# Kernel tuning notes

Measured on AMD Instinct MI355X. Metric: run time of the kernel, lower is better.

## Reference

```python
import jax, jax.numpy as jnp
import numpy as np

TRUNC = 2.0  # NSFP truncated chamfer: squared dists >= 2 are zeroed


def _mlp(x, W0, b0, Wh, bh, Wl, bl):
    h = jax.nn.relu(x @ W0 + b0)
    for i in range(Wh.shape[0]):
        h = jax.nn.relu(h @ Wh[i] + bh[i])
    return h @ Wl + bl


def _chamfer(x, y):
    d = (jnp.sum(x * x, axis=1)[:, None]
         + jnp.sum(y * y, axis=1)[None, :]
         - 2.0 * (x @ y.T))
    dx = jnp.min(d, axis=1)  # [N] NN dist x->y
    dy = jnp.min(d, axis=0)  # [M] NN dist y->x
    dx = jnp.where(dx < TRUNC, dx, 0.0)
    dy = jnp.where(dy < TRUNC, dy, 0.0)
    return jnp.mean(dx) + jnp.mean(dy)


def setup_inputs() -> dict:
    key = jax.random.key(0)
    ks = jax.random.split(key, 16)
    N = 20000
    F = 128
    H = 7  # hidden 128->128 layers (layer_size=8)
    s_in = 1.0 / np.sqrt(3.0)
    s_h = 1.0 / np.sqrt(F)
    d = {
        'pc0': jax.random.normal(ks[0], (N, 3), jnp.float32) * 10.0,
        'pc1': jax.random.normal(ks[1], (N, 3), jnp.float32) * 10.0,
        'W0': jax.random.normal(ks[2], (3, F), jnp.float32) * s_in,
        'b0': jnp.zeros((F,), jnp.float32),
        'Wh': jax.random.normal(ks[3], (H, F, F), jnp.float32) * s_h,
        'bh': jnp.zeros((H, F), jnp.float32),
        'Wl': jax.random.normal(ks[4], (F, 3), jnp.float32) * s_h,
        'bl': jnp.zeros((3,), jnp.float32),
        'W0i': jax.random.normal(ks[5], (3, F), jnp.float32) * s_in,
        'b0i': jnp.zeros((F,), jnp.float32),
        'Whi': jax.random.normal(ks[6], (H, F, F), jnp.float32) * s_h,
        'bhi': jnp.zeros((H, F), jnp.float32),
        'Wli': jax.random.normal(ks[7], (F, 3), jnp.float32) * s_h,
        'bli': jnp.zeros((3,), jnp.float32),
    }
    return d


def reference(pc0, pc1, W0, b0, Wh, bh, Wl, bl,
              W0i, b0i, Whi, bhi, Wli, bli):
    forward_flow = _mlp(pc0, W0, b0, Wh, bh, Wl, bl)          # [N,3]
    pc0_to_pc1 = pc0 + forward_flow
    inverse_flow = _mlp(pc0_to_pc1, W0i, b0i, Whi, bhi, Wli, bli)
    est_pc1_to_pc0 = pc0_to_pc1 - inverse_flow
    forward_loss = _chamfer(pc0_to_pc1, pc1)
    inverse_loss = _chamfer(est_pc1_to_pc0, pc0)
    return forward_loss + inverse_loss


if __name__ == '__main__':
    out = reference(**setup_inputs())
    print(out)
```

## Files before the change

### kernel.cpp

```cpp
#include <hip/hip_runtime.h>
#include <hip/hip_bf16.h>

#define F 128
#define NHID 7
#define BP 80
#define NPT 5
#define TRUNC_ 2.0f

#define GM 32
#define GM3 (GM * GM * GM)
#define GLO (-28.0f)
#define CELL 1.75f
#define GINV (1.0f / 1.75f)
#define SCAN_BLKS (GM3 / 256)
#define NGRID 4
#define PACKB 896
#define ZB (NGRID * GM3 / 256)
#define BQ 128

typedef __attribute__((ext_vector_type(8))) short short8v;
typedef __attribute__((ext_vector_type(4))) float f32x4;

__device__ inline unsigned short f2bf(float v)
{
    __hip_bfloat16 b = __float2bfloat16(v);
    return __builtin_bit_cast(unsigned short, b);
}
__device__ inline float bf2f(unsigned short u)
{
    unsigned int x = ((unsigned int)u) << 16;
    return __builtin_bit_cast(float, x);
}

__device__ inline int hsw(int row, int col)
{
    return row * 128 + ((((col >> 3) ^ (row & 7)) << 3) | (col & 7));
}

__device__ inline void barrier_nd()
{
    asm volatile("s_waitcnt lgkmcnt(0)" ::: "memory");
    __builtin_amdgcn_s_barrier();
}

__global__ __launch_bounds__(256) void prep_kernel(
    const float* __restrict__ Wh, const float* __restrict__ Whi,
    const float* __restrict__ Wl, const float* __restrict__ Wli,
    unsigned short* __restrict__ whp, unsigned short* __restrict__ wlp,
    float* __restrict__ wlt, int* __restrict__ counts, unsigned int* __restrict__ done)
{
    int bid = blockIdx.x;
    int t = threadIdx.x;
    if (bid < PACKB) {
        int idx = bid * 256 + t;
        int j = idx & 7;
        int l = (idx >> 3) & 63;
        int tt = (idx >> 9) & 7;
        int s = (idx >> 12) & 3;
        int m = idx >> 14;
        int k = s * 32 + (l >> 4) * 8 + j;
        int c = tt * 16 + (l & 15);
        const float* W = (m < 7 ? Wh + (size_t)m * F * F
                                : Whi + (size_t)(m - 7) * F * F);
        float w = W[k * F + c];
        unsigned short hi = f2bf(w);
        unsigned short lo = f2bf(w - bf2f(hi));
        whp[idx] = hi;
        wlp[idx] = lo;
    } else if (bid < PACKB + ZB) {
        counts[(bid - PACKB) * 256 + t] = 0;
    } else {
#pragma unroll
        for (int r = 0; r < 3; ++r) {
            int e = r * 256 + t;
            int mI = e / 384;
            int rem = e - mI * 384;
            int c = rem >> 7;
            int k = rem & 127;
            const float* W = mI ? Wli : Wl;
            wlt[e] = W[k * 3 + c];
        }
        if (t == 0) *done = 0u;
    }
}

__device__ inline int cell_of(float x, float y, float z)
{
    int cx = (int)floorf((x - GLO) * GINV);
    int cy = (int)floorf((y - GLO) * GINV);
    int cz = (int)floorf((z - GLO) * GINV);
    cx = min(max(cx, 0), GM - 1);
    cy = min(max(cy, 0), GM - 1);
    cz = min(max(cz, 0), GM - 1);
    return (cz * GM + cy) * GM + cx;
}

__global__ __launch_bounds__(512, 2) void mlp_fused_kernel(
    const float* __restrict__ pc0, const float* __restrict__ pc1,
    const float* __restrict__ W0a, const float* __restrict__ b0a,
    const float* __restrict__ W0b, const float* __restrict__ b0b,
    const unsigned short* __restrict__ whp,
    const unsigned short* __restrict__ wlp,
    const float* __restrict__ bha, const float* __restrict__ bhb,
    const float* __restrict__ wlt,
    const float* __restrict__ bla, const float* __restrict__ blb,
    float* __restrict__ Aout, float* __restrict__ Cout,
    int* __restrict__ counts, int N)
{
    __shared__ unsigned short hX[BP * 128];
    __shared__ unsigned short hY[BP * 128];
    __shared__ float Al[BP][4];
    __shared__ float Cl[BP][4];

    const int tid = threadIdx.x;
    const int lane = tid & 63;
    const int wv = tid >> 6;
    const int arow = lane & 15;
    const int kg = lane >> 4;
    const int p0 = blockIdx.x * BP;

    unsigned short* cur = hX;
    unsigned short* nxt = hY;

    short8v wAhi, wAlo, wBhi, wBlo;
    short8v hA[NPT], hB[NPT];

#define LW(WHI, WLO, LI, S) { \
        size_t off = ((size_t)(((LI) * 4 + (S)) * 8 + wv) * 64 + lane) * 8; \
        WHI = *(const short8v*)(whp + off); \
        WLO = *(const short8v*)(wlp + off); }
#define LH(D, S) { _Pragma("unroll") for (int p = 0; p < NPT; ++p) \
        D[p] = *(const short8v*)&cur[hsw(p * 16 + arow, (S) * 32 + kg * 8)]; }
#define MM(WHI, WLO, H) { \
    _Pragma("unroll") for (int p = 0; p < NPT; ++p) \
        acc[p] = __builtin_amdgcn_mfma_f32_16x16x32_bf16(WHI, H[p], acc[p], 0, 0, 0); \
    _Pragma("unroll") for (int p = 0; p < NPT; ++p) \
        acc[p] = __builtin_amdgcn_mfma_f32_16x16x32_bf16(WLO, H[p], acc[p], 0, 0, 0); }

    LW(wAhi, wAlo, 0, 0)
    LW(wBhi, wBlo, 0, 1)
    __builtin_amdgcn_sched_barrier(0);

    for (int M = 0; M < 2; ++M) {
        const float* W0 = M ? W0b : W0a;
        const float* b0 = M ? b0b : b0a;
        const float* bh = M ? bhb : bha;
        const float* bl = M ? blb : bla;

        {
            const int jg = tid & 31;
            const int pgg = tid >> 5;
            const int j0 = jg * 4;
            float4 wr0 = *(const float4*)(W0 + 0 * F + j0);
            float4 wr1 = *(const float4*)(W0 + 1 * F + j0);
            float4 wr2 = *(const float4*)(W0 + 2 * F + j0);
            float4 bb0 = *(const float4*)(b0 + j0);
#pragma unroll
            for (int p = 0; p < 5; ++p) {
                int pt = pgg * 5 + p;
                float x0, x1, x2;
                if (M == 0) {
                    int gp = p0 + pt;
                    int cp = gp < N ? gp : N - 1;
                    x0 = pc0[cp * 3 + 0]; x1 = pc0[cp * 3 + 1]; x2 = pc0[cp * 3 + 2];
                } else {
                    x0 = Al[pt][0]; x1 = Al[pt][1]; x2 = Al[pt][2];
                }
                float hx = fmaxf(fmaf(x0, wr0.x, fmaf(x1, wr1.x, fmaf(x2, wr2.x, bb0.x))), 0.f);
                float hy = fmaxf(fmaf(x0, wr0.y, fmaf(x1, wr1.y, fmaf(x2, wr2.y, bb0.y))), 0.f);
                float hz = fmaxf(fmaf(x0, wr0.z, fmaf(x1, wr1.z, fmaf(x2, wr2.z, bb0.z))), 0.f);
                float hw = fmaxf(fmaf(x0, wr0.w, fmaf(x1, wr1.w, fmaf(x2, wr2.w, bb0.w))), 0.f);
                short4 hv = make_short4((short)f2bf(hx), (short)f2bf(hy),
                                        (short)f2bf(hz), (short)f2bf(hw));
                *(short4*)&cur[hsw(pt, j0)] = hv;
            }
        }
        barrier_nd();

        for (int l = 0; l < NHID; ++l) {
            const int L = M * 7 + l;
            const int Ln = (L + 1 < 14) ? (L + 1) : 13;
            f32x4 acc[NPT];
            {
                float4 b4 = *(const float4*)&bh[l * F + wv * 16 + kg * 4];
#pragma unroll
                for (int p = 0; p < NPT; ++p)
                    acc[p] = (f32x4){b4.x, b4.y, b4.z, b4.w};
            }

            LH(hA, 0) LH(hB, 1)
            __builtin_amdgcn_sched_barrier(0);
            MM(wAhi, wAlo, hA)
            LW(wAhi, wAlo, L, 2) LH(hA, 2)
            __builtin_amdgcn_sched_barrier(0);
            MM(wBhi, wBlo, hB)
            LW(wBhi, wBlo, L, 3) LH(hB, 3)
            __builtin_amdgcn_sched_barrier(0);
            MM(wAhi, wAlo, hA)
            LW(wAhi, wAlo, Ln, 0)
            __builtin_amdgcn_sched_barrier(0);
            MM(wBhi, wBlo, hB)
            LW(wBhi, wBlo, Ln, 1)

#pragma unroll
            for (int p = 0; p < NPT; ++p) {
                float v0 = fmaxf(acc[p][0], 0.f), v1 = fmaxf(acc[p][1], 0.f);
                float v2 = fmaxf(acc[p][2], 0.f), v3 = fmaxf(acc[p][3], 0.f);
                short4 hv = make_short4((short)f2bf(v0), (short)f2bf(v1),
                                        (short)f2bf(v2), (short)f2bf(v3));
                *(short4*)&nxt[hsw(p * 16 + arow, wv * 16 + kg * 4)] = hv;
            }
            barrier_nd();
            unsigned short* tsw = cur; cur = nxt; nxt = tsw;
        }

        if (tid < 240) {
            int pt = tid / 3;
            int c = tid - 3 * pt;
            const float* wl = wlt + M * 384 + c * 128;
            float a0 = 0.f, a1 = 0.f, a2 = 0.f, a3 = 0.f;
#pragma unroll
            for (int q = 0; q < 16; ++q) {
                short8v h8 = *(const short8v*)&cur[hsw(pt, q * 8)];
                float4 wa = *(const float4*)(wl + q * 8);
                float4 wb = *(const float4*)(wl + q * 8 + 4);
                a0 = fmaf(bf2f((unsigned short)h8[0]), wa.x, a0);
                a1 = fmaf(bf2f((unsigned short)h8[1]), wa.y, a1);
                a2 = fmaf(bf2f((unsigned short)h8[2]), wa.z, a2);
                a3 = fmaf(bf2f((unsigned short)h8[3]), wa.w, a3);
                a0 = fmaf(bf2f((unsigned short)h8[4]), wb.x, a0);
                a1 = fmaf(bf2f((unsigned short)h8[5]), wb.y, a1);
                a2 = fmaf(bf2f((unsigned short)h8[6]), wb.z, a2);
                a3 = fmaf(bf2f((unsigned short)h8[7]), wb.w, a3);
            }
            float flow = ((a0 + a1) + (a2 + a3)) + bl[c];
            int gp = p0 + pt;
            int cp = gp < N ? gp : N - 1;
            if (M == 0) {
                float val = pc0[cp * 3 + c] + flow;
                Al[pt][c] = val;
                if (gp < N) Aout[gp * 3 + c] = val;
            } else {
                float val = Al[pt][c] - flow;
                Cl[pt][c] = val;
                if (gp < N) Cout[gp * 3 + c] = val;
            }
        }
        barrier_nd();
    }
#undef LW
#undef LH
#undef MM

    if (tid < BP) {
        int gp = p0 + tid;
        if (gp < N) {
            atomicAdd(&counts[1 * GM3 + cell_of(Al[tid][0], Al[tid][1], Al[tid][2])], 1);
            atomicAdd(&counts[3 * GM3 + cell_of(Cl[tid][0], Cl[tid][1], Cl[tid][2])], 1);
            atomicAdd(&counts[0 * GM3 + cell_of(pc1[gp * 3 + 0], pc1[gp * 3 + 1], pc1[gp * 3 + 2])], 1);
            atomicAdd(&counts[2 * GM3 + cell_of(pc0[gp * 3 + 0], pc0[gp * 3 + 1], pc0[gp * 3 + 2])], 1);
        }
    }
}

__device__ inline const float* cloud_ptr(int g, const float* g0, const float* g1,
                                         const float* g2, const float* g3)
{
    return g == 0 ? g0 : (g == 1 ? g1 : (g == 2 ? g2 : g3));
}

__global__ __launch_bounds__(256) void scan1(
    const int* __restrict__ counts, int* __restrict__ offs, int* __restrict__ bsum)
{
    int tid = threadIdx.x;
    int i = blockIdx.x * 256 + tid;
    int v = counts[i];
    __shared__ int s[256];
    s[tid] = v;
    __syncthreads();
#pragma unroll
    for (int off = 1; off < 256; off <<= 1) {
        int t = (tid >= off) ? s[tid - off] : 0;
        __syncthreads();
        s[tid] += t;
        __syncthreads();
    }
    offs[i] = s[tid] - v;
    if (tid == 255) bsum[blockIdx.x] = s[255];
}

__global__ __launch_bounds__(256) void scan23(
    int* __restrict__ offs, const int* __restrict__ bsum, int* __restrict__ counts)
{
    int seg = blockIdx.x / SCAN_BLKS;
    int pos = blockIdx.x - seg * SCAN_BLKS;
    const int* bs = bsum + seg * SCAN_BLKS;
    int t = threadIdx.x;
    int v = (t < pos) ? bs[t] : 0;
    __shared__ int red[4];
#pragma unroll
    for (int o = 32; o > 0; o >>= 1) v += __shfl_down(v, o, 64);
    if ((t & 63) == 0) red[t >> 6] = v;
    __syncthreads();
    int prefix = red[0] + red[1] + red[2] + red[3];
    int i = blockIdx.x * 256 + t;
    offs[i] += prefix;
    counts[i] = 0;
}

__global__ __launch_bounds__(256) void grid_fill(
    const float* __restrict__ B, const float* __restrict__ A,
    const float* __restrict__ D, const float* __restrict__ C,
    const int* __restrict__ offs, int* __restrict__ counts,
    float4* __restrict__ pts, int n)
{
    int g = blockIdx.y;
    const float* P = cloud_ptr(g, B, A, D, C);
    int i = blockIdx.x * 256 + threadIdx.x;
    if (i < n) {
        float x = P[i * 3 + 0], y = P[i * 3 + 1], z = P[i * 3 + 2];
        int c = g * GM3 + cell_of(x, y, z);
        int slot = offs[c] + atomicAdd(&counts[c], 1);
        pts[(size_t)g * n + slot] = make_float4(x, y, z, 0.f);
    }
}

__device__ inline float block_sum256(float v)
{
    __shared__ float sws[4];
#pragma unroll
    for (int o = 32; o > 0; o >>= 1) v += __shfl_down(v, o, 64);
    int w = threadIdx.x >> 6;
    if ((threadIdx.x & 63) == 0) sws[w] = v;
    __syncthreads();
    if (threadIdx.x == 0) v = sws[0] + sws[1] + sws[2] + sws[3];
    return v;
}

__device__ inline float boxd1(float q, int c)
{
    float lo = GLO + c * CELL;
    return fmaxf(fmaxf(lo - q, q - (lo + CELL)), 0.f);
}

__global__ __launch_bounds__(256) void grid_search(
    const int* __restrict__ offs, const int* __restrict__ counts,
    const float4* __restrict__ pts, float* __restrict__ partials,
    unsigned int* __restrict__ done, float* __restrict__ out, float inv, int n)
{
    const int d = blockIdx.y;
    const float4* Qs = pts + (size_t)(d ^ 1) * n;
    const float4* P  = pts + (size_t)d * n;
    const int* ofs = offs + (size_t)d * GM3;
    const int* cnt = counts + (size_t)d * GM3;

    const int tid = threadIdx.x;
    const int ql = tid & (BQ - 1);
    const int half = tid >> 7;
    const int i = blockIdx.x * BQ + ql;

    float mn = 3.4e38f;
    if (i < n) {
        float4 q = Qs[i];
        int cx = min(max((int)floorf((q.x - GLO) * GINV), 0), GM - 1);
        int cy = min(max((int)floorf((q.y - GLO) * GINV), 0), GM - 1);
        int cz = min(max((int)floorf((q.z - GLO) * GINV), 0), GM - 1);
        int xcl = max(cx - 1, 0), xch = min(cx + 1, GM - 1);
        int r0 = half * 4;

        int o[5], e[5];
#pragma unroll
        for (int r = 0; r < 5; ++r) {
            o[r] = 0; e[r] = 0;
            bool act = half ? true : (r < 4);
            if (act) {
                int rr = r0 + r;
                int dz = rr / 3, dy = rr - dz * 3;
                int z = cz + dz - 1;
                int y = cy + dy - 1;
                if ((unsigned)z < GM && (unsigned)y < GM) {
                    float dzd = boxd1(q.z, z);
                    float dyd = boxd1(q.y, y);
                    float dyz2 = fmaf(dzd, dzd, dyd * dyd);
                    if (dyz2 < TRUNC_) {
                        float rx = sqrtf(TRUNC_ - dyz2);
                        int xlo = max((int)floorf((q.x - rx - GLO) * GINV), xcl);
                        int xhi = min((int)floorf((q.x + rx - GLO) * GINV), xch);
                        if (xlo <= xhi) {
                            int rowbase = (z * GM + y) * GM;
                            o[r] = ofs[rowbase + xlo];
                            e[r] = ofs[rowbase + xhi] + cnt[rowbase + xhi];
                        }
                    }
                }
            }
        }
#pragma unroll
        for (int r = 0; r < 5; ++r) {
            for (int k = o[r]; k < e[r]; ++k) {
                float4 p = P[k];
                float ddx = q.x - p.x, ddy = q.y - p.y, ddz = q.z - p.z;
                mn = fminf(mn, fmaf(ddx, ddx, fmaf(ddy, ddy, ddz * ddz)));
            }
        }
    }

    __shared__ float m0[BQ];
    if (half == 0) m0[ql] = mn;
    __syncthreads();
    float val = 0.f;
    if (half == 1 && i < n) {
        float m = fminf(mn, m0[ql]);
        val = (m < TRUNC_) ? m : 0.f;
    }
    float bs = block_sum256(val);

    __shared__ int lastflag;
    if (threadIdx.x == 0) {
        atomicExch(&partials[(size_t)d * gridDim.x + blockIdx.x], bs);
        __threadfence();
        unsigned v = atomicAdd(done, 1u);
        lastflag = (v == (unsigned)(NGRID * gridDim.x - 1)) ? 1 : 0;
    }
    __syncthreads();
    if (lastflag) {
        int NPt = NGRID * gridDim.x;
        float s = 0.f;
        for (int j = threadIdx.x; j < NPt; j += 256)
            s += atomicAdd(&partials[j], 0.0f);
        __syncthreads();
        float tot = block_sum256(s);
        if (threadIdx.x == 0) out[0] = tot * inv;
    }
}

extern "C" void kernel_launch(void* const* d_in, const int* in_sizes, int n_in,
                              void* d_out, int out_size, void* d_ws, size_t ws_size,
                              hipStream_t stream)
{
    const float* pc0 = (const float*)d_in[0];
    const float* pc1 = (const float*)d_in[1];
    const float* W0  = (const float*)d_in[2];
    const float* b0  = (const float*)d_in[3];
    const float* Wh  = (const float*)d_in[4];
    const float* bh  = (const float*)d_in[5];
    const float* Wl  = (const float*)d_in[6];
    const float* bl  = (const float*)d_in[7];
    const float* W0i = (const float*)d_in[8];
    const float* b0i = (const float*)d_in[9];
    const float* Whi = (const float*)d_in[10];
    const float* bhi = (const float*)d_in[11];
    const float* Wli = (const float*)d_in[12];
    const float* bli = (const float*)d_in[13];
    float* out = (float*)d_out;

    const int N = in_sizes[0] / 3;

    char* base = (char*)d_ws;
    float*  A        = (float*)(base + 0);
    float*  C        = (float*)(base + 240000);
    int*    counts   = (int*)  (base + 480000);
    int*    offs     = (int*)  (base + 1004288);
    int*    bsum     = (int*)  (base + 1528576);
    float4* pts      = (float4*)(base + 1532672);
    float*  partials = (float*)(base + 2812672);
    unsigned int* done = (unsigned int*)(base + 2816768);
    unsigned short* whp = (unsigned short*)(base + 2816784);
    unsigned short* wlp = (unsigned short*)(base + 3275536);
    float*  wlt      = (float*)(base + 3734288);

    const int PB = (N + 255) / 256;
    const int QB = (N + BQ - 1) / BQ;

    hipLaunchKernelGGL(prep_kernel, dim3(PACKB + ZB + 1), dim3(256), 0, stream,
                       Wh, Whi, Wl, Wli, whp, wlp, wlt, counts, done);

    int mlpg = (N + BP - 1) / BP;
    hipLaunchKernelGGL(mlp_fused_kernel, dim3(mlpg), dim3(512), 0, stream,
                       pc0, pc1, W0, b0, W0i, b0i, whp, wlp, bh, bhi,
                       wlt, bl, bli, A, C, counts, N);

    hipLaunchKernelGGL(scan1, dim3(ZB), dim3(256), 0, stream, counts, offs, bsum);
    hipLaunchKernelGGL(scan23, dim3(ZB), dim3(256), 0, stream, offs, bsum, counts);
    hipLaunchKernelGGL(grid_fill, dim3(PB, NGRID), dim3(256), 0, stream,
                       pc1, A, pc0, C, offs, counts, pts, N);

    hipLaunchKernelGGL(grid_search, dim3(QB, NGRID), dim3(256), 0, stream,
                       offs, counts, pts, partials, done, out,
                       1.0f / (float)N, N);
}
```

Measured before the change: 78.54 us.

## Fuse scan, grid fill and grid search into one persistent kernel with grid barriers

Replaces the four post-MLP kernels (two-stage scan, grid fill, neighbour search) with a single kernel whose phases are separated by software grid-wide barriers built on atomic counters. The aim is to remove three kernel launches and the idle gaps between dependent stages. In exchange, all 4*QB blocks must be resident at once or the spin barriers deadlock, and every barrier adds spin and fence overhead. Launch bounds request three blocks per CU to make co-residency more likely.

```diff
diff --git a/kernel.cpp b/kernel.cpp
--- a/kernel.cpp
+++ b/kernel.cpp
@@ -43,11 +43,24 @@
     __builtin_amdgcn_s_barrier();
 }
 
+__device__ inline void gbar(unsigned int* ctr, unsigned int target)
+{
+    __syncthreads();
+    if (threadIdx.x == 0) {
+        __threadfence();
+        atomicAdd(ctr, 1u);
+        while (atomicAdd(ctr, 0u) < target)
+            __builtin_amdgcn_s_sleep(4);
+        __threadfence();
+    }
+    __syncthreads();
+}
+
 __global__ __launch_bounds__(256) void prep_kernel(
     const float* __restrict__ Wh, const float* __restrict__ Whi,
     const float* __restrict__ Wl, const float* __restrict__ Wli,
     unsigned short* __restrict__ whp, unsigned short* __restrict__ wlp,
-    float* __restrict__ wlt, int* __restrict__ counts, unsigned int* __restrict__ done)
+    float* __restrict__ wlt, int* __restrict__ counts, unsigned int* __restrict__ syncv)
 {
     int bid = blockIdx.x;
     int t = threadIdx.x;
@@ -80,7 +93,7 @@
             const float* W = mI ? Wli : Wl;
             wlt[e] = W[k * 3 + c];
         }
-        if (t == 0) *done = 0u;
+        if (t < 8) syncv[t] = 0u;
     }
 }
 
@@ -269,62 +282,6 @@
     return g == 0 ? g0 : (g == 1 ? g1 : (g == 2 ? g2 : g3));
 }
 
-__global__ __launch_bounds__(256) void scan1(
-    const int* __restrict__ counts, int* __restrict__ offs, int* __restrict__ bsum)
-{
-    int tid = threadIdx.x;
-    int i = blockIdx.x * 256 + tid;
-    int v = counts[i];
-    __shared__ int s[256];
-    s[tid] = v;
-    __syncthreads();
-#pragma unroll
-    for (int off = 1; off < 256; off <<= 1) {
-        int t = (tid >= off) ? s[tid - off] : 0;
-        __syncthreads();
-        s[tid] += t;
-        __syncthreads();
-    }
-    offs[i] = s[tid] - v;
-    if (tid == 255) bsum[blockIdx.x] = s[255];
-}
-
-__global__ __launch_bounds__(256) void scan23(
-    int* __restrict__ offs, const int* __restrict__ bsum, int* __restrict__ counts)
-{
-    int seg = blockIdx.x / SCAN_BLKS;
-    int pos = blockIdx.x - seg * SCAN_BLKS;
-    const int* bs = bsum + seg * SCAN_BLKS;
-    int t = threadIdx.x;
-    int v = (t < pos) ? bs[t] : 0;
-    __shared__ int red[4];
-#pragma unroll
-    for (int o = 32; o > 0; o >>= 1) v += __shfl_down(v, o, 64);
-    if ((t & 63) == 0) red[t >> 6] = v;
-    __syncthreads();
-    int prefix = red[0] + red[1] + red[2] + red[3];
-    int i = blockIdx.x * 256 + t;
-    offs[i] += prefix;
-    counts[i] = 0;
-}
-
-__global__ __launch_bounds__(256) void grid_fill(
-    const float* __restrict__ B, const float* __restrict__ A,
-    const float* __restrict__ D, const float* __restrict__ C,
-    const int* __restrict__ offs, int* __restrict__ counts,
-    float4* __restrict__ pts, int n)
-{
-    int g = blockIdx.y;
-    const float* P = cloud_ptr(g, B, A, D, C);
-    int i = blockIdx.x * 256 + threadIdx.x;
-    if (i < n) {
-        float x = P[i * 3 + 0], y = P[i * 3 + 1], z = P[i * 3 + 2];
-        int c = g * GM3 + cell_of(x, y, z);
-        int slot = offs[c] + atomicAdd(&counts[c], 1);
-        pts[(size_t)g * n + slot] = make_float4(x, y, z, 0.f);
-    }
-}
-
 __device__ inline float block_sum256(float v)
 {
     __shared__ float sws[4];
@@ -343,94 +300,153 @@
     return fmaxf(fmaxf(lo - q, q - (lo + CELL)), 0.f);
 }
 
-__global__ __launch_bounds__(256) void grid_search(
-    const int* __restrict__ offs, const int* __restrict__ counts,
-    const float4* __restrict__ pts, float* __restrict__ partials,
-    unsigned int* __restrict__ done, float* __restrict__ out, float inv, int n)
-{
-    const int d = blockIdx.y;
-    const float4* Qs = pts + (size_t)(d ^ 1) * n;
-    const float4* P  = pts + (size_t)d * n;
-    const int* ofs = offs + (size_t)d * GM3;
-    const int* cnt = counts + (size_t)d * GM3;
-
-    const int tid = threadIdx.x;
-    const int ql = tid & (BQ - 1);
-    const int half = tid >> 7;
-    const int i = blockIdx.x * BQ + ql;
-
-    float mn = 3.4e38f;
-    if (i < n) {
-        float4 q = Qs[i];
-        int cx = min(max((int)floorf((q.x - GLO) * GINV), 0), GM - 1);
-        int cy = min(max((int)floorf((q.y - GLO) * GINV), 0), GM - 1);
-        int cz = min(max((int)floorf((q.z - GLO) * GINV), 0), GM - 1);
-        int xcl = max(cx - 1, 0), xch = min(cx + 1, GM - 1);
-        int r0 = half * 4;
-
-        int o[5], e[5];
-#pragma unroll
-        for (int r = 0; r < 5; ++r) {
-            o[r] = 0; e[r] = 0;
-            bool act = half ? true : (r < 4);
-            if (act) {
-                int rr = r0 + r;
-                int dz = rr / 3, dy = rr - dz * 3;
-                int z = cz + dz - 1;
-                int y = cy + dy - 1;
-                if ((unsigned)z < GM && (unsigned)y < GM) {
-                    float dzd = boxd1(q.z, z);
-                    float dyd = boxd1(q.y, y);
-                    float dyz2 = fmaf(dzd, dzd, dyd * dyd);
-                    if (dyz2 < TRUNC_) {
-                        float rx = sqrtf(TRUNC_ - dyz2);
-                        int xlo = max((int)floorf((q.x - rx - GLO) * GINV), xcl);
-                        int xhi = min((int)floorf((q.x + rx - GLO) * GINV), xch);
-                        if (xlo <= xhi) {
-                            int rowbase = (z * GM + y) * GM;
-                            o[r] = ofs[rowbase + xlo];
-                            e[r] = ofs[rowbase + xhi] + cnt[rowbase + xhi];
+__global__ __launch_bounds__(256, 3) void grid_pipeline(
+    const float* __restrict__ Bc, const float* __restrict__ Ac,
+    const float* __restrict__ Dc, const float* __restrict__ Cc,
+    int* __restrict__ offs, int* __restrict__ counts, int* __restrict__ bsum,
+    float4* __restrict__ pts, float* __restrict__ partials,
+    unsigned int* __restrict__ syncv, float* __restrict__ out, float inv, int n)
+{
+    const int bid = blockIdx.x;
+    const int t = threadIdx.x;
+    const unsigned int GPB = gridDim.x;
+    const int QB = (n + BQ - 1) / BQ;
+    const int PB = (n + 255) / 256;
+
+    __shared__ int s[256];
+    __shared__ float m0[BQ];
+    __shared__ int lastflag;
+
+    if (bid < ZB) {
+        int i = bid * 256 + t;
+        int v = counts[i];
+        s[t] = v;
+        __syncthreads();
+#pragma unroll
+        for (int off = 1; off < 256; off <<= 1) {
+            int x = (t >= off) ? s[t - off] : 0;
+            __syncthreads();
+            s[t] += x;
+            __syncthreads();
+        }
+        offs[i] = s[t] - v;
+        if (t == 255) bsum[bid] = s[255];
+    }
+    gbar(&syncv[0], GPB);
+
+    if (bid < ZB) {
+        int seg = bid / SCAN_BLKS;
+        int pos = bid - seg * SCAN_BLKS;
+        const int* bs = bsum + seg * SCAN_BLKS;
+        int v = (t < pos) ? bs[t] : 0;
+        __shared__ int red[4];
+#pragma unroll
+        for (int o = 32; o > 0; o >>= 1) v += __shfl_down(v, o, 64);
+        if ((t & 63) == 0) red[t >> 6] = v;
+        __syncthreads();
+        int prefix = red[0] + red[1] + red[2] + red[3];
+        int i = bid * 256 + t;
+        offs[i] += prefix;
+        counts[i] = 0;
+    }
+    gbar(&syncv[1], GPB);
+
+    if (bid < PB * NGRID) {
+        int g = bid / PB;
+        int xb = bid - g * PB;
+        const float* P = cloud_ptr(g, Bc, Ac, Dc, Cc);
+        int i = xb * 256 + t;
+        if (i < n) {
+            float x = P[i * 3 + 0], y = P[i * 3 + 1], z = P[i * 3 + 2];
+            int c = g * GM3 + cell_of(x, y, z);
+            int slot = offs[c] + atomicAdd(&counts[c], 1);
+            pts[(size_t)g * n + slot] = make_float4(x, y, z, 0.f);
+        }
+    }
+    gbar(&syncv[2], GPB);
+
+    {
+        const int d = bid / QB;
+        const int qb = bid - d * QB;
+        const float4* Qs = pts + (size_t)(d ^ 1) * n;
+        const float4* P  = pts + (size_t)d * n;
+        const int* ofs = offs + (size_t)d * GM3;
+        const int* cnt = counts + (size_t)d * GM3;
+
+        const int ql = t & (BQ - 1);
+        const int half = t >> 7;
+        const int i = qb * BQ + ql;
+
+        float mn = 3.4e38f;
+        if (i < n) {
+            float4 q = Qs[i];
+            int cx = min(max((int)floorf((q.x - GLO) * GINV), 0), GM - 1);
+            int cy = min(max((int)floorf((q.y - GLO) * GINV), 0), GM - 1);
+            int cz = min(max((int)floorf((q.z - GLO) * GINV), 0), GM - 1);
+            int xcl = max(cx - 1, 0), xch = min(cx + 1, GM - 1);
+            int r0 = half * 4;
+
+            int o[5], e[5];
+#pragma unroll
+            for (int r = 0; r < 5; ++r) {
+                o[r] = 0; e[r] = 0;
+                bool act = half ? true : (r < 4);
+                if (act) {
+                    int rr = r0 + r;
+                    int dz = rr / 3, dy = rr - dz * 3;
+                    int z = cz + dz - 1;
+                    int y = cy + dy - 1;
+                    if ((unsigned)z < GM && (unsigned)y < GM) {
+                        float dzd = boxd1(q.z, z);
+                        float dyd = boxd1(q.y, y);
+                        float dyz2 = fmaf(dzd, dzd, dyd * dyd);
+                        if (dyz2 < TRUNC_) {
+                            float rx = sqrtf(TRUNC_ - dyz2);
+                            int xlo = max((int)floorf((q.x - rx - GLO) * GINV), xcl);
+                            int xhi = min((int)floorf((q.x + rx - GLO) * GINV), xch);
+                            if (xlo <= xhi) {
+                                int rowbase = (z * GM + y) * GM;
+                                o[r] = ofs[rowbase + xlo];
+                                e[r] = ofs[rowbase + xhi] + cnt[rowbase + xhi];
+                            }
                         }
                     }
                 }
             }
-        }
-#pragma unroll
-        for (int r = 0; r < 5; ++r) {
-            for (int k = o[r]; k < e[r]; ++k) {
-                float4 p = P[k];
-                float ddx = q.x - p.x, ddy = q.y - p.y, ddz = q.z - p.z;
-                mn = fminf(mn, fmaf(ddx, ddx, fmaf(ddy, ddy, ddz * ddz)));
-            }
-        }
-    }
-
-    __shared__ float m0[BQ];
-    if (half == 0) m0[ql] = mn;
-    __syncthreads();
-    float val = 0.f;
-    if (half == 1 && i < n) {
-        float m = fminf(mn, m0[ql]);
-        val = (m < TRUNC_) ? m : 0.f;
-    }
-    float bs = block_sum256(val);
-
-    __shared__ int lastflag;
-    if (threadIdx.x == 0) {
-        atomicExch(&partials[(size_t)d * gridDim.x + blockIdx.x], bs);
-        __threadfence();
-        unsigned v = atomicAdd(done, 1u);
-        lastflag = (v == (unsigned)(NGRID * gridDim.x - 1)) ? 1 : 0;
-    }
-    __syncthreads();
-    if (lastflag) {
-        int NPt = NGRID * gridDim.x;
-        float s = 0.f;
-        for (int j = threadIdx.x; j < NPt; j += 256)
-            s += atomicAdd(&partials[j], 0.0f);
+#pragma unroll
+            for (int r = 0; r < 5; ++r) {
+                for (int k = o[r]; k < e[r]; ++k) {
+                    float4 p = P[k];
+                    float ddx = q.x - p.x, ddy = q.y - p.y, ddz = q.z - p.z;
+                    mn = fminf(mn, fmaf(ddx, ddx, fmaf(ddy, ddy, ddz * ddz)));
+                }
+            }
+        }
+
+        if (half == 0) m0[ql] = mn;
         __syncthreads();
-        float tot = block_sum256(s);
-        if (threadIdx.x == 0) out[0] = tot * inv;
+        float val = 0.f;
+        if (half == 1 && i < n) {
+            float m = fminf(mn, m0[ql]);
+            val = (m < TRUNC_) ? m : 0.f;
+        }
+        float bs = block_sum256(val);
+
+        if (t == 0) {
+            atomicExch(&partials[bid], bs);
+            __threadfence();
+            unsigned v = atomicAdd(&syncv[3], 1u);
+            lastflag = (v == GPB - 1u) ? 1 : 0;
+        }
+        __syncthreads();
+        if (lastflag) {
+            float ss = 0.f;
+            for (int j = t; j < (int)GPB; j += 256)
+                ss += atomicAdd(&partials[j], 0.0f);
+            __syncthreads();
+            float tot = block_sum256(ss);
+            if (t == 0) out[0] = tot * inv;
+        }
     }
 }
 
@@ -464,28 +480,22 @@
     int*    bsum     = (int*)  (base + 1528576);
     float4* pts      = (float4*)(base + 1532672);
     float*  partials = (float*)(base + 2812672);
-    unsigned int* done = (unsigned int*)(base + 2816768);
-    unsigned short* whp = (unsigned short*)(base + 2816784);
-    unsigned short* wlp = (unsigned short*)(base + 3275536);
-    float*  wlt      = (float*)(base + 3734288);
-
-    const int PB = (N + 255) / 256;
+    unsigned int* syncv = (unsigned int*)(base + 2816768);
+    unsigned short* whp = (unsigned short*)(base + 2816800);
+    unsigned short* wlp = (unsigned short*)(base + 3275552);
+    float*  wlt      = (float*)(base + 3734304);
+
     const int QB = (N + BQ - 1) / BQ;
 
     hipLaunchKernelGGL(prep_kernel, dim3(PACKB + ZB + 1), dim3(256), 0, stream,
-                       Wh, Whi, Wl, Wli, whp, wlp, wlt, counts, done);
+                       Wh, Whi, Wl, Wli, whp, wlp, wlt, counts, syncv);
 
     int mlpg = (N + BP - 1) / BP;
     hipLaunchKernelGGL(mlp_fused_kernel, dim3(mlpg), dim3(512), 0, stream,
                        pc0, pc1, W0, b0, W0i, b0i, whp, wlp, bh, bhi,
                        wlt, bl, bli, A, C, counts, N);
 
-    hipLaunchKernelGGL(scan1, dim3(ZB), dim3(256), 0, stream, counts, offs, bsum);
-    hipLaunchKernelGGL(scan23, dim3(ZB), dim3(256), 0, stream, offs, bsum, counts);
-    hipLaunchKernelGGL(grid_fill, dim3(PB, NGRID), dim3(256), 0, stream,
-                       pc1, A, pc0, C, offs, counts, pts, N);
-
-    hipLaunchKernelGGL(grid_search, dim3(QB, NGRID), dim3(256), 0, stream,
-                       offs, counts, pts, partials, done, out,
-                       1.0f / (float)N, N);
-}
+    hipLaunchKernelGGL(grid_pipeline, dim3(NGRID * QB), dim3(256), 0, stream,
+                       pc1, A, pc0, C, offs, counts, bsum, pts, partials,
+                       syncv, out, 1.0f / (float)N, N);
+}
```

Measured after the change: 244.8 us. 212% more time.

## Double-buffer full-layer MLP weights and split grid search into four sub-threads per query

Applied to the files above, without the earlier changes.

The MLP kernel now double-buffers all four weight slices of the next layer in registers, prefetching them during the current layer's MFMAs and fully unrolling the layer loops, so weight-load latency is hidden across layers. The grid search assigns four threads per query (3+2+2+2 cell rows) instead of two, which doubles the number of blocks and shortens the per-thread serial neighbor scan. The partials buffer grows, so the workspace offsets shift. The cost is more register pressure in the MLP kernel, which may reduce occupancy or spill, and a larger reduction in the grid search.

```diff
diff --git a/kernel.cpp b/kernel.cpp
--- a/kernel.cpp
+++ b/kernel.cpp
@@ -16,7 +16,7 @@
 #define NGRID 4
 #define PACKB 896
 #define ZB (NGRID * GM3 / 256)
-#define BQ 128
+#define QPB 64
 
 typedef __attribute__((ext_vector_type(8))) short short8v;
 typedef __attribute__((ext_vector_type(4))) float f32x4;
@@ -122,25 +122,25 @@
     unsigned short* cur = hX;
     unsigned short* nxt = hY;
 
-    short8v wAhi, wAlo, wBhi, wBlo;
+    short8v whB[2][4], wlB[2][4];
     short8v hA[NPT], hB[NPT];
 
-#define LW(WHI, WLO, LI, S) { \
+#define LWB(NB, LI, S) { \
         size_t off = ((size_t)(((LI) * 4 + (S)) * 8 + wv) * 64 + lane) * 8; \
-        WHI = *(const short8v*)(whp + off); \
-        WLO = *(const short8v*)(wlp + off); }
+        whB[NB][S] = *(const short8v*)(whp + off); \
+        wlB[NB][S] = *(const short8v*)(wlp + off); }
 #define LH(D, S) { _Pragma("unroll") for (int p = 0; p < NPT; ++p) \
         D[p] = *(const short8v*)&cur[hsw(p * 16 + arow, (S) * 32 + kg * 8)]; }
-#define MM(WHI, WLO, H) { \
+#define MMB(B, S, H) { \
     _Pragma("unroll") for (int p = 0; p < NPT; ++p) \
-        acc[p] = __builtin_amdgcn_mfma_f32_16x16x32_bf16(WHI, H[p], acc[p], 0, 0, 0); \
+        acc[p] = __builtin_amdgcn_mfma_f32_16x16x32_bf16(whB[B][S], H[p], acc[p], 0, 0, 0); \
     _Pragma("unroll") for (int p = 0; p < NPT; ++p) \
-        acc[p] = __builtin_amdgcn_mfma_f32_16x16x32_bf16(WLO, H[p], acc[p], 0, 0, 0); }
-
-    LW(wAhi, wAlo, 0, 0)
-    LW(wBhi, wBlo, 0, 1)
+        acc[p] = __builtin_amdgcn_mfma_f32_16x16x32_bf16(wlB[B][S], H[p], acc[p], 0, 0, 0); }
+
+    LWB(0, 0, 0) LWB(0, 0, 1) LWB(0, 0, 2) LWB(0, 0, 3)
     __builtin_amdgcn_sched_barrier(0);
 
+#pragma unroll
     for (int M = 0; M < 2; ++M) {
         const float* W0 = M ? W0b : W0a;
         const float* b0 = M ? b0b : b0a;
@@ -177,8 +177,11 @@
         }
         barrier_nd();
 
+#pragma unroll
         for (int l = 0; l < NHID; ++l) {
             const int L = M * 7 + l;
+            const int b = L & 1;
+            const int nb = b ^ 1;
             const int Ln = (L + 1 < 14) ? (L + 1) : 13;
             f32x4 acc[NPT];
             {
@@ -190,17 +193,17 @@
 
             LH(hA, 0) LH(hB, 1)
             __builtin_amdgcn_sched_barrier(0);
-            MM(wAhi, wAlo, hA)
-            LW(wAhi, wAlo, L, 2) LH(hA, 2)
+            MMB(b, 0, hA)
+            LH(hA, 2)
+            LWB(nb, Ln, 0) LWB(nb, Ln, 1)
             __builtin_amdgcn_sched_barrier(0);
-            MM(wBhi, wBlo, hB)
-            LW(wBhi, wBlo, L, 3) LH(hB, 3)
+            MMB(b, 1, hB)
+            LH(hB, 3)
+            LWB(nb, Ln, 2) LWB(nb, Ln, 3)
             __builtin_amdgcn_sched_barrier(0);
-            MM(wAhi, wAlo, hA)
-            LW(wAhi, wAlo, Ln, 0)
+            MMB(b, 2, hA)
             __builtin_amdgcn_sched_barrier(0);
-            MM(wBhi, wBlo, hB)
-            LW(wBhi, wBlo, Ln, 1)
+            MMB(b, 3, hB)
 
 #pragma unroll
             for (int p = 0; p < NPT; ++p) {
@@ -248,9 +251,9 @@
         }
         barrier_nd();
     }
-#undef LW
+#undef LWB
 #undef LH
-#undef MM
+#undef MMB
 
     if (tid < BP) {
         int gp = p0 + tid;
@@ -354,10 +357,10 @@
     const int* ofs = offs + (size_t)d * GM3;
     const int* cnt = counts + (size_t)d * GM3;
 
-    const int tid = threadIdx.x;
-    const int ql = tid & (BQ - 1);
-    const int half = tid >> 7;
-    const int i = blockIdx.x * BQ + ql;
+    const int t = threadIdx.x;
+    const int ql = t & (QPB - 1);
+    const int sub = t >> 6;
+    const int i = blockIdx.x * QPB + ql;
 
     float mn = 3.4e38f;
     if (i < n) {
@@ -366,15 +369,15 @@
         int cy = min(max((int)floorf((q.y - GLO) * GINV), 0), GM - 1);
         int cz = min(max((int)floorf((q.z - GLO) * GINV), 0), GM - 1);
         int xcl = max(cx - 1, 0), xch = min(cx + 1, GM - 1);
-        int r0 = half * 4;
-
-        int o[5], e[5];
-#pragma unroll
-        for (int r = 0; r < 5; ++r) {
+        int rbase = (sub == 0) ? 0 : (2 * sub + 1);
+        int rcnt = (sub == 0) ? 3 : 2;
+
+        int o[3], e[3];
+#pragma unroll
+        for (int r = 0; r < 3; ++r) {
             o[r] = 0; e[r] = 0;
-            bool act = half ? true : (r < 4);
-            if (act) {
-                int rr = r0 + r;
+            if (r < rcnt) {
+                int rr = rbase + r;
                 int dz = rr / 3, dy = rr - dz * 3;
                 int z = cz + dz - 1;
                 int y = cy + dy - 1;
@@ -396,7 +399,7 @@
             }
         }
 #pragma unroll
-        for (int r = 0; r < 5; ++r) {
+        for (int r = 0; r < 3; ++r) {
             for (int k = o[r]; k < e[r]; ++k) {
                 float4 p = P[k];
                 float ddx = q.x - p.x, ddy = q.y - p.y, ddz = q.z - p.z;
@@ -405,18 +408,18 @@
         }
     }
 
-    __shared__ float m0[BQ];
-    if (half == 0) m0[ql] = mn;
+    __shared__ float m4[3][QPB];
+    if (sub) m4[sub - 1][ql] = mn;
     __syncthreads();
     float val = 0.f;
-    if (half == 1 && i < n) {
-        float m = fminf(mn, m0[ql]);
+    if (sub == 0 && i < n) {
+        float m = fminf(fminf(mn, m4[0][ql]), fminf(m4[1][ql], m4[2][ql]));
         val = (m < TRUNC_) ? m : 0.f;
     }
     float bs = block_sum256(val);
 
     __shared__ int lastflag;
-    if (threadIdx.x == 0) {
+    if (t == 0) {
         atomicExch(&partials[(size_t)d * gridDim.x + blockIdx.x], bs);
         __threadfence();
         unsigned v = atomicAdd(done, 1u);
@@ -426,11 +429,11 @@
     if (lastflag) {
         int NPt = NGRID * gridDim.x;
         float s = 0.f;
-        for (int j = threadIdx.x; j < NPt; j += 256)
+        for (int j = t; j < NPt; j += 256)
             s += atomicAdd(&partials[j], 0.0f);
         __syncthreads();
         float tot = block_sum256(s);
-        if (threadIdx.x == 0) out[0] = tot * inv;
+        if (t == 0) out[0] = tot * inv;
     }
 }
 
@@ -464,13 +467,13 @@
     int*    bsum     = (int*)  (base + 1528576);
     float4* pts      = (float4*)(base + 1532672);
     float*  partials = (float*)(base + 2812672);
-    unsigned int* done = (unsigned int*)(base + 2816768);
-    unsigned short* whp = (unsigned short*)(base + 2816784);
-    unsigned short* wlp = (unsigned short*)(base + 3275536);
-    float*  wlt      = (float*)(base + 3734288);
+    unsigned int* done = (unsigned int*)(base + 2820864);
+    unsigned short* whp = (unsigned short*)(base + 2820880);
+    unsigned short* wlp = (unsigned short*)(base + 3279632);
+    float*  wlt      = (float*)(base + 3738384);
 
     const int PB = (N + 255) / 256;
-    const int QB = (N + BQ - 1) / BQ;
+    const int QB = (N + QPB - 1) / QPB;
 
     hipLaunchKernelGGL(prep_kernel, dim3(PACKB + ZB + 1), dim3(256), 0, stream,
                        Wh, Whi, Wl, Wli, whp, wlp, wlt, counts, done);
```

After: 85.00 us. 8.2% more time.
